# Kernel tuning notes

Measured on AMD Instinct MI355X. Metric: run time of the kernel, lower is better.

The kernel has to match this reference:

```python
import jax, jax.numpy as jnp
import numpy as np

EPS = 1e-6
NUM_HEADS = 8
ATTN_DIM = 64
LINEAR_DIM = 64


def _layer_norm(x, eps=EPS):
    # F.layer_norm without elementwise affine
    mu = jnp.mean(x, axis=-1, keepdims=True)
    var = jnp.mean(jnp.square(x - mu), axis=-1, keepdims=True)
    return (x - mu) * jax.lax.rsqrt(var + eps)


def setup_inputs() -> dict:
    key = jax.random.key(0)
    k1, k2, k3 = jax.random.split(key, 3)
    B, N, D = 4, 2048, 512
    x = jax.random.normal(k1, (B, N, D), dtype=jnp.float32)
    invalid_attn_mask = jnp.tril(jnp.ones((N, N), dtype=jnp.float32))  # causal
    uvqk = jax.random.normal(k2, (D, 2 * LINEAR_DIM * NUM_HEADS + 2 * ATTN_DIM * NUM_HEADS), dtype=jnp.float32) * 0.02
    o_w = jax.random.normal(k3, (D, LINEAR_DIM * NUM_HEADS), dtype=jnp.float32) * (1.0 / np.sqrt(D))  # torch Linear weight [out, in]
    o_b = jnp.zeros((D,), dtype=jnp.float32)
    return {"x": x, "invalid_attn_mask": invalid_attn_mask, "uvqk": uvqk, "o_w": o_w, "o_b": o_b}


def reference(x, invalid_attn_mask, uvqk, o_w, o_b):
    B, N, D = x.shape
    H, dA, dL = NUM_HEADS, ATTN_DIM, LINEAR_DIM
    normed_x = _layer_norm(x)
    # fused uvqk projection + silu activation
    proj = jax.nn.silu(jnp.einsum('bnd,de->bne', normed_x, uvqk))
    u, v, q, k = jnp.split(proj, [dL * H, 2 * dL * H, 2 * dL * H + dA * H], axis=-1)
    q_h = q.reshape(B, N, H, dA)
    k_h = k.reshape(B, N, H, dA)
    v_h = v.reshape(B, N, H, dL)
    # HSTU attention: SiLU(qk)/N, then mask multiply (no softmax)
    qk_attn = jnp.einsum('bnhd,bmhd->bhnm', q_h, k_h)
    qk_attn = jax.nn.silu(qk_attn) / N
    qk_attn = qk_attn * invalid_attn_mask[None, None, :, :]
    attn = jnp.einsum('bhnm,bmhd->bnhd', qk_attn, v_h).reshape(B, N, H * dL)
    a = _layer_norm(attn)
    o_input = u * a
    out = jnp.einsum('bnf,df->bnd', o_input, o_w) + o_b + x
    return out
```

## Files before the change

kernel.cpp:

```cpp
#include <hip/hip_runtime.h>
#include <cstdint>

#define NTOK 2048
#define DIM 512
#define EDIM 2048
#define BATCH 4
#define HEADS 8
#define BNROWS 8192
#define INV_N (1.0f/2048.0f)

typedef unsigned short u16;
typedef __bf16 bf16x8 __attribute__((ext_vector_type(8)));
typedef u16   u16x8  __attribute__((ext_vector_type(8)));
typedef u16   u16x4  __attribute__((ext_vector_type(4)));
typedef float f32x4  __attribute__((ext_vector_type(4)));

__device__ __forceinline__ u16 f2bf(float f) {
  union { float f; uint32_t u; } v; v.f = f;
  uint32_t r = v.u + 0x7FFFu + ((v.u >> 16) & 1u);
  return (u16)(r >> 16);
}
__device__ __forceinline__ u16 f2bfc(float f) {
  return __builtin_bit_cast(u16, (__bf16)f);
}
__device__ __forceinline__ float bf2f(u16 b) {
  union { uint32_t u; float f; } v; v.u = ((uint32_t)b) << 16;
  return v.f;
}
__device__ __forceinline__ bf16x8 ldb(const u16* p) {
  u16x8 r = *(const u16x8*)p;
  return __builtin_bit_cast(bf16x8, r);
}
#define MFMA16(a,b,c) __builtin_amdgcn_mfma_f32_16x16x32_bf16((a),(b),(c),0,0,0)

__device__ __forceinline__ float silu_nr(float s) {
  float e = __expf(-s);
  e = fminf(e, 1.7e38f);
  float d = 1.0f + e;
  float r = __builtin_amdgcn_rcpf(d);
  r = r * fmaf(-d, r, 2.0f);
  return s * r;
}

__device__ __forceinline__ void gload16(const u16* g, u16* lds) {
  __builtin_amdgcn_global_load_lds(
      (const __attribute__((address_space(1))) void*)g,
      (__attribute__((address_space(3))) void*)lds, 16, 0, 0);
}

__global__ __launch_bounds__(256) void k_pre(const float* __restrict__ uvqk,
                                             const float* __restrict__ ow,
                                             const float* __restrict__ x,
                                             u16* __restrict__ uvqk_t,
                                             u16* __restrict__ ow_bf,
                                             u16* __restrict__ xn) {
  __shared__ float tile[32][33];
  int bid = blockIdx.x, tid = threadIdx.x;
  if (bid < 1024) {
    int tx = tid & 31, ty = tid >> 5;
    int j0 = (bid & 63) * 32, k0 = (bid >> 6) * 32;
#pragma unroll
    for (int r = ty; r < 32; r += 8)
      tile[r][tx] = uvqk[(size_t)(k0 + r) * EDIM + j0 + tx];
    __syncthreads();
#pragma unroll
    for (int r = ty; r < 32; r += 8)
      uvqk_t[(size_t)(j0 + r) * DIM + k0 + tx] = f2bfc(tile[tx][r]);
  } else if (bid < 1280) {
    int i4 = (bid - 1024) * 1024 + tid * 4;
    float4 v = *(const float4*)(ow + i4);
    u16x4 o = {f2bfc(v.x), f2bfc(v.y), f2bfc(v.z), f2bfc(v.w)};
    *(u16x4*)(ow_bf + i4) = o;
  } else {
    int lane = tid & 63, wid = tid >> 6;
    size_t row = (size_t)(bid - 1280) * 4 + wid;
    const float* xr = x + row * DIM;
    float4 a = ((const float4*)xr)[lane * 2];
    float4 b = ((const float4*)xr)[lane * 2 + 1];
    float s = a.x + a.y + a.z + a.w + b.x + b.y + b.z + b.w;
#pragma unroll
    for (int o = 32; o; o >>= 1) s += __shfl_xor(s, o);
    float mu = s * (1.0f / DIM);
    float d[8] = {a.x - mu, a.y - mu, a.z - mu, a.w - mu,
                  b.x - mu, b.y - mu, b.z - mu, b.w - mu};
    float v = 0.f;
#pragma unroll
    for (int j = 0; j < 8; ++j) v += d[j] * d[j];
#pragma unroll
    for (int o = 32; o; o >>= 1) v += __shfl_xor(v, o);
    float rs = rsqrtf(v * (1.0f / DIM) + 1e-6f);
    u16x8 o8;
#pragma unroll
    for (int j = 0; j < 8; ++j) o8[j] = f2bfc(d[j] * rs);
    *(u16x8*)(xn + row * DIM + lane * 8) = o8;
  }
}

__global__ __launch_bounds__(256) void k_gemm1(const u16* __restrict__ A,
                                               const u16* __restrict__ Bt,
                                               u16* __restrict__ P,
                                               u16* __restrict__ vt) {
  __shared__ u16 As[128 * 64];
  __shared__ u16 Bs[128 * 64];
  int tid = threadIdx.x, lane = tid & 63, wid = tid >> 6;
  int lm = lane & 15, lg = lane >> 4;
  int wr = wid >> 1, wc = wid & 1;

  int bid = blockIdx.x;
  int xcd = bid & 7, idx = bid >> 3;
  int orig = xcd * 128 + idx;
  int r0 = (orig >> 4) * 128;
  int c0 = (orig & 15) * 128;

  int srow = wid * 8 + (lane >> 3);
  int scol = (lane & 7) * 8;

  f32x4 acc[4][4];
  f32x4 z = {0.f, 0.f, 0.f, 0.f};
#pragma unroll
  for (int mt = 0; mt < 4; ++mt)
#pragma unroll
    for (int nt = 0; nt < 4; ++nt) acc[mt][nt] = z;

  for (int ks = 0; ks < DIM / 64; ++ks) {
#pragma unroll
    for (int it = 0; it < 4; ++it) {
      gload16(A + (size_t)(r0 + it * 32 + srow) * DIM + ks * 64 + scol,
              As + it * 2048 + wid * 512);
      gload16(Bt + (size_t)(c0 + it * 32 + srow) * DIM + ks * 64 + scol,
              Bs + it * 2048 + wid * 512);
    }
    __syncthreads();

#pragma unroll
    for (int kk = 0; kk < 2; ++kk) {
      bf16x8 am[4], bn[4];
#pragma unroll
      for (int mt = 0; mt < 4; ++mt)
        am[mt] = ldb(&As[(wr * 64 + mt * 16 + lm) * 64 + kk * 32 + lg * 8]);
#pragma unroll
      for (int nt = 0; nt < 4; ++nt)
        bn[nt] = ldb(&Bs[(wc * 64 + nt * 16 + lm) * 64 + kk * 32 + lg * 8]);
#pragma unroll
      for (int mt = 0; mt < 4; ++mt)
#pragma unroll
        for (int nt = 0; nt < 4; ++nt)
          acc[mt][nt] = MFMA16(am[mt], bn[nt], acc[mt][nt]);
    }
    __syncthreads();
  }

  bool isv = (c0 >= 512) && (c0 < 1024);
  int btc = r0 >> 11;
  int nbw = (r0 & 2047) + wr * 64;
  int hv  = ((c0 - 512) >> 6) + wc;

  u16* ws = ((wid >> 1) ? Bs : As) + (wid & 1) * 4096;

#pragma unroll
  for (int mt = 0; mt < 4; ++mt)
#pragma unroll
    for (int nt = 0; nt < 4; ++nt) {
      u16 pv[4];
#pragma unroll
      for (int i = 0; i < 4; ++i) {
        pv[i] = f2bfc(silu_nr(acc[mt][nt][i]));
        int row = mt * 16 + lg * 4 + i;
        int col = nt * 16 + lm;
        ws[row * 64 + (col ^ ((row & 7) << 3))] = pv[i];
      }
      if (isv) {
        int e = nt * 16 + lm;
        int n = nbw + mt * 16 + lg * 4;
        u16x4 pk = {pv[0], pv[1], pv[2], pv[3]};
        *(u16x4*)(vt + ((size_t)(btc * 8 + hv) * 64 + e) * NTOK + n) = pk;
      }
    }

#pragma unroll
  for (int p = 0; p < 8; ++p) {
    int rrow = p * 8 + (lane >> 3);
    int rcol = (lane & 7) * 8;
    u16x8 vv = *(const u16x8*)&ws[rrow * 64 + (rcol ^ ((rrow & 7) << 3))];
    *(u16x8*)(P + (size_t)(r0 + wr * 64 + rrow) * EDIM + c0 + wc * 64 + rcol) = vv;
  }
}

__global__ __launch_bounds__(256) void k_attn(const u16* __restrict__ proj,
                                              const u16* __restrict__ vt,
                                              float* __restrict__ attn) {
  __shared__ u16 kv0[8192];
  __shared__ u16 kv1[8192];
  __shared__ u16 p_lds[4][16][64];
  int tid = threadIdx.x, lane = tid & 63, w = tid >> 6;
  int lm = lane & 15, lg = lane >> 4;

  int bid = blockIdx.x;
  int xcd = bid & 7, idx = bid >> 3;
  int qtile = 31 - (idx >> 2);
  int bh = (xcd << 2) + (idx & 3);
  int b = bh >> 3, h = bh & 7;
  int n0 = qtile * 64;
  int nrow = n0 + w * 16;
  int nlm = nrow + lm;

  const u16* pb = proj + (size_t)b * NTOK * EDIM;
  const u16* kb = pb + 1536 + h * 64;
  const u16* vb = vt + (size_t)bh * 64 * NTOK;

  f32x4 z = {0.f, 0.f, 0.f, 0.f};

  int sr = lane >> 3;
  int sc = ((lane & 7) ^ sr) * 8;
  const u16* ks0 = kb + (size_t)(w * 16 + sr) * EDIM + sc;
  const u16* ks1 = kb + (size_t)(w * 16 + 8 + sr) * EDIM + sc;
  const u16* vs0 = vb + (size_t)(w * 16 + sr) * NTOK + sc;
  const u16* vs1 = vb + (size_t)(w * 16 + 8 + sr) * NTOK + sc;

  const u16* qrow = pb + (size_t)nlm * EDIM + 1024 + h * 64 + lg * 8;
  bf16x8 qf0 = ldb(qrow), qf1 = ldb(qrow + 32);

  f32x4 acc[4];
#pragma unroll
  for (int et = 0; et < 4; ++et) acc[et] = z;

  int psw = (lm & 7) << 3;

  gload16(ks0, kv0 + (w * 16) * 64);
  gload16(ks1, kv0 + (w * 16 + 8) * 64);
  gload16(vs0, kv0 + 4096 + (w * 16) * 64);
  gload16(vs1, kv0 + 4096 + (w * 16 + 8) * 64);
  asm volatile("s_waitcnt vmcnt(0)" ::: "memory");
  __builtin_amdgcn_s_barrier();

  int ntl = qtile + 1;
  for (int t = 0; t < ntl; ++t) {
    const u16* kt = (t & 1) ? kv1 : kv0;
    const u16* vl = kt + 4096;
    if (t + 1 < ntl) {
      u16* kd = ((t + 1) & 1) ? kv1 : kv0;
      size_t ko = (size_t)(t + 1) * 64 * EDIM;
      size_t vo = (size_t)(t + 1) * 64;
      gload16(ks0 + ko, kd + (w * 16) * 64);
      gload16(ks1 + ko, kd + (w * 16 + 8) * 64);
      gload16(vs0 + vo, kd + 4096 + (w * 16) * 64);
      gload16(vs1 + vo, kd + 4096 + (w * 16 + 8) * 64);
    }
    bf16x8 kf[4][2];
#pragma unroll
    for (int mb = 0; mb < 4; ++mb)
#pragma unroll
      for (int kk = 0; kk < 2; ++kk)
        kf[mb][kk] = ldb(&kt[(mb * 16 + lm) * 64 +
                             ((kk * 32 + lg * 8) ^ ((lm & 7) << 3))]);
    if (t == qtile) {
#pragma unroll
      for (int mb = 0; mb < 4; ++mb) {
        f32x4 s = MFMA16(kf[mb][0], qf0, z);
        s = MFMA16(kf[mb][1], qf1, s);
        int m = t * 64 + mb * 16 + lg * 4;
        u16x4 pk;
#pragma unroll
        for (int i = 0; i < 4; ++i)
          pk[i] = (m + i <= nlm) ? f2bfc(silu_nr(s[i])) : (u16)0;
        *(u16x4*)&p_lds[w][lm][(mb * 16 + lg * 4) ^ psw] = pk;
      }
    } else {
#pragma unroll
      for (int mb = 0; mb < 4; ++mb) {
        f32x4 s = MFMA16(kf[mb][0], qf0, z);
        s = MFMA16(kf[mb][1], qf1, s);
        u16x4 pk;
#pragma unroll
        for (int i = 0; i < 4; ++i) pk[i] = f2bfc(silu_nr(s[i]));
        *(u16x4*)&p_lds[w][lm][(mb * 16 + lg * 4) ^ psw] = pk;
      }
    }
    bf16x8 vf[2][4];
#pragma unroll
    for (int kk = 0; kk < 2; ++kk)
#pragma unroll
      for (int et = 0; et < 4; ++et)
        vf[kk][et] = ldb(&vl[(et * 16 + lm) * 64 +
                             ((kk * 32 + lg * 8) ^ ((lm & 7) << 3))]);
    bf16x8 pf0 = ldb(&p_lds[w][lm][(lg * 8) ^ psw]);
    bf16x8 pf1 = ldb(&p_lds[w][lm][(32 + lg * 8) ^ psw]);
#pragma unroll
    for (int et = 0; et < 4; ++et) {
      acc[et] = MFMA16(pf0, vf[0][et], acc[et]);
      acc[et] = MFMA16(pf1, vf[1][et], acc[et]);
    }
    asm volatile("s_waitcnt vmcnt(0)" ::: "memory");
    __builtin_amdgcn_s_barrier();
  }

#pragma unroll
  for (int et = 0; et < 4; ++et)
#pragma unroll
    for (int i = 0; i < 4; ++i)
      attn[((size_t)b * NTOK + nrow + lg * 4 + i) * DIM +
           h * 64 + et * 16 + lm] = acc[et][i] * INV_N;
}

__global__ __launch_bounds__(256) void k_gemm2f(const float* __restrict__ attn,
                                                const u16* __restrict__ proj,
                                                const u16* __restrict__ Bw,
                                                const float* __restrict__ o_b,
                                                const float* __restrict__ x,
                                                float* __restrict__ out) {
  __shared__ u16 os[32 * 512];
  int tid = threadIdx.x, lane = tid & 63, w = tid >> 6;
  int lm = lane & 15, lg = lane >> 4;

  int bid = blockIdx.x;
  int xcd = bid & 7, idx = bid >> 3;
  int r0 = (xcd * 32 + idx) * 32;

#pragma unroll
  for (int rr = 0; rr < 8; ++rr) {
    int r = w * 8 + rr;
    const float* ar = attn + (size_t)(r0 + r) * DIM;
    float4 a = ((const float4*)ar)[lane * 2];
    float4 b = ((const float4*)ar)[lane * 2 + 1];
    float s = a.x + a.y + a.z + a.w + b.x + b.y + b.z + b.w;
#pragma unroll
    for (int o = 32; o; o >>= 1) s += __shfl_xor(s, o);
    float mu = s * (1.0f / DIM);
    float d[8] = {a.x - mu, a.y - mu, a.z - mu, a.w - mu,
                  b.x - mu, b.y - mu, b.z - mu, b.w - mu};
    float v = 0.f;
#pragma unroll
    for (int j = 0; j < 8; ++j) v += d[j] * d[j];
#pragma unroll
    for (int o = 32; o; o >>= 1) v += __shfl_xor(v, o);
    float rs = rsqrtf(v * (1.0f / DIM) + 1e-6f);
    u16x8 u8 = *(const u16x8*)(proj + (size_t)(r0 + r) * EDIM + lane * 8);
    u16x8 o8;
#pragma unroll
    for (int j = 0; j < 8; ++j) o8[j] = f2bf(bf2f(u8[j]) * (d[j] * rs));
    *(u16x8*)&os[r * 512 + ((lane * 8) ^ ((r & 7) << 3))] = o8;
  }
  __syncthreads();

  int cb = w * 128;
  f32x4 acc[2][8];
  f32x4 z = {0.f, 0.f, 0.f, 0.f};
#pragma unroll
  for (int mt = 0; mt < 2; ++mt)
#pragma unroll
    for (int nt = 0; nt < 8; ++nt) acc[mt][nt] = z;

#pragma unroll 2
  for (int kc = 0; kc < 16; ++kc) {
    bf16x8 af[2];
#pragma unroll
    for (int mt = 0; mt < 2; ++mt)
      af[mt] = ldb(&os[(mt * 16 + lm) * 512 +
                       ((kc * 32 + lg * 8) ^ ((lm & 7) << 3))]);
    bf16x8 bfr[8];
#pragma unroll
    for (int nt = 0; nt < 8; ++nt)
      bfr[nt] = ldb(Bw + (size_t)(cb + nt * 16 + lm) * DIM + kc * 32 + lg * 8);
#pragma unroll
    for (int mt = 0; mt < 2; ++mt)
#pragma unroll
      for (int nt = 0; nt < 8; ++nt)
        acc[mt][nt] = MFMA16(af[mt], bfr[nt], acc[mt][nt]);
  }

#pragma unroll
  for (int mt = 0; mt < 2; ++mt)
#pragma unroll
    for (int nt = 0; nt < 8; ++nt)
#pragma unroll
      for (int i = 0; i < 4; ++i) {
        size_t row = r0 + mt * 16 + lg * 4 + i;
        int col = cb + nt * 16 + lm;
        out[row * DIM + col] = acc[mt][nt][i] + o_b[col] + x[row * DIM + col];
      }
}

extern "C" void kernel_launch(void* const* d_in, const int* in_sizes, int n_in,
                              void* d_out, int out_size, void* d_ws, size_t ws_size,
                              hipStream_t stream) {
  const float* x    = (const float*)d_in[0];
  const float* uvqk = (const float*)d_in[2];
  const float* o_w  = (const float*)d_in[3];
  const float* o_b  = (const float*)d_in[4];
  float* out = (float*)d_out;

  u16* uvqk_t = (u16*)d_ws;
  u16* ow_bf  = uvqk_t + (size_t)EDIM * DIM;
  u16* xn     = ow_bf + (size_t)DIM * DIM;
  u16* proj   = xn + (size_t)BNROWS * DIM;
  float* attn = (float*)(proj + (size_t)BNROWS * EDIM);
  u16* o_in   = (u16*)(attn + (size_t)BNROWS * DIM);
  u16* vt     = o_in + (size_t)BNROWS * DIM;

  k_pre<<<dim3(3328), 256, 0, stream>>>(uvqk, o_w, x, uvqk_t, ow_bf, xn);
  k_gemm1<<<dim3(1024), 256, 0, stream>>>(xn, uvqk_t, proj, vt);
  k_attn<<<dim3(1024), 256, 0, stream>>>(proj, vt, attn);
  k_gemm2f<<<dim3(256), 256, 0, stream>>>(attn, proj, ow_bf, o_b, x, out);
}
```

Before: 112.6 us.

## Pair causal query tiles per attention block and halve gemm2 row tile

The attention kernel now processes 128-row query tiles, with each wave handling two 16-row sub-tiles. Each block runs two paired tiles (qt and 15-qt), so every block gets the same causal work and each K/V tile loaded into LDS is reused by more queries. MFMA priority is raised around the PV accumulation. The output GEMM drops to 16-row tiles and 512 blocks to raise parallelism, at the cost of reloading the o_w fragments more often.

```diff
diff --git a/kernel.cpp b/kernel.cpp
--- a/kernel.cpp
+++ b/kernel.cpp
@@ -191,18 +191,15 @@
                                               float* __restrict__ attn) {
   __shared__ u16 kv0[8192];
   __shared__ u16 kv1[8192];
-  __shared__ u16 p_lds[4][16][64];
+  __shared__ u16 p_lds[4][2][16][64];
   int tid = threadIdx.x, lane = tid & 63, w = tid >> 6;
   int lm = lane & 15, lg = lane >> 4;
 
   int bid = blockIdx.x;
   int xcd = bid & 7, idx = bid >> 3;
-  int qtile = 31 - (idx >> 2);
-  int bh = (xcd << 2) + (idx & 3);
+  int bh = (xcd << 2) + (idx >> 4);
+  int pairp = idx & 15;
   int b = bh >> 3, h = bh & 7;
-  int n0 = qtile * 64;
-  int nrow = n0 + w * 16;
-  int nlm = nrow + lm;
 
   const u16* pb = proj + (size_t)b * NTOK * EDIM;
   const u16* kb = pb + 1536 + h * 64;
@@ -217,89 +214,120 @@
   const u16* vs0 = vb + (size_t)(w * 16 + sr) * NTOK + sc;
   const u16* vs1 = vb + (size_t)(w * 16 + 8 + sr) * NTOK + sc;
 
-  const u16* qrow = pb + (size_t)nlm * EDIM + 1024 + h * 64 + lg * 8;
-  bf16x8 qf0 = ldb(qrow), qf1 = ldb(qrow + 32);
-
-  f32x4 acc[4];
-#pragma unroll
-  for (int et = 0; et < 4; ++et) acc[et] = z;
-
   int psw = (lm & 7) << 3;
 
-  gload16(ks0, kv0 + (w * 16) * 64);
-  gload16(ks1, kv0 + (w * 16 + 8) * 64);
-  gload16(vs0, kv0 + 4096 + (w * 16) * 64);
-  gload16(vs1, kv0 + 4096 + (w * 16 + 8) * 64);
-  asm volatile("s_waitcnt vmcnt(0)" ::: "memory");
-  __builtin_amdgcn_s_barrier();
-
-  int ntl = qtile + 1;
-  for (int t = 0; t < ntl; ++t) {
-    const u16* kt = (t & 1) ? kv1 : kv0;
-    const u16* vl = kt + 4096;
-    if (t + 1 < ntl) {
-      u16* kd = ((t + 1) & 1) ? kv1 : kv0;
-      size_t ko = (size_t)(t + 1) * 64 * EDIM;
-      size_t vo = (size_t)(t + 1) * 64;
-      gload16(ks0 + ko, kd + (w * 16) * 64);
-      gload16(ks1 + ko, kd + (w * 16 + 8) * 64);
-      gload16(vs0 + vo, kd + 4096 + (w * 16) * 64);
-      gload16(vs1 + vo, kd + 4096 + (w * 16 + 8) * 64);
-    }
-    bf16x8 kf[4][2];
-#pragma unroll
-    for (int mb = 0; mb < 4; ++mb)
-#pragma unroll
-      for (int kk = 0; kk < 2; ++kk)
-        kf[mb][kk] = ldb(&kt[(mb * 16 + lm) * 64 +
-                             ((kk * 32 + lg * 8) ^ ((lm & 7) << 3))]);
-    if (t == qtile) {
-#pragma unroll
-      for (int mb = 0; mb < 4; ++mb) {
-        f32x4 s = MFMA16(kf[mb][0], qf0, z);
-        s = MFMA16(kf[mb][1], qf1, s);
-        int m = t * 64 + mb * 16 + lg * 4;
-        u16x4 pk;
-#pragma unroll
-        for (int i = 0; i < 4; ++i)
-          pk[i] = (m + i <= nlm) ? f2bfc(silu_nr(s[i])) : (u16)0;
-        *(u16x4*)&p_lds[w][lm][(mb * 16 + lg * 4) ^ psw] = pk;
-      }
-    } else {
-#pragma unroll
-      for (int mb = 0; mb < 4; ++mb) {
-        f32x4 s = MFMA16(kf[mb][0], qf0, z);
-        s = MFMA16(kf[mb][1], qf1, s);
-        u16x4 pk;
-#pragma unroll
-        for (int i = 0; i < 4; ++i) pk[i] = f2bfc(silu_nr(s[i]));
-        *(u16x4*)&p_lds[w][lm][(mb * 16 + lg * 4) ^ psw] = pk;
-      }
-    }
-    bf16x8 vf[2][4];
-#pragma unroll
-    for (int kk = 0; kk < 2; ++kk)
-#pragma unroll
-      for (int et = 0; et < 4; ++et)
-        vf[kk][et] = ldb(&vl[(et * 16 + lm) * 64 +
-                             ((kk * 32 + lg * 8) ^ ((lm & 7) << 3))]);
-    bf16x8 pf0 = ldb(&p_lds[w][lm][(lg * 8) ^ psw]);
-    bf16x8 pf1 = ldb(&p_lds[w][lm][(32 + lg * 8) ^ psw]);
-#pragma unroll
-    for (int et = 0; et < 4; ++et) {
-      acc[et] = MFMA16(pf0, vf[0][et], acc[et]);
-      acc[et] = MFMA16(pf1, vf[1][et], acc[et]);
-    }
+#pragma unroll
+  for (int ph = 0; ph < 2; ++ph) {
+    int qt = ph ? pairp : (15 - pairp);
+    int n0 = qt * 128;
+    int nw = n0 + w * 32;
+
+    bf16x8 qf[2][2];
+#pragma unroll
+    for (int qs = 0; qs < 2; ++qs) {
+      const u16* qrow = pb + (size_t)(nw + qs * 16 + lm) * EDIM + 1024 + h * 64 + lg * 8;
+      qf[qs][0] = ldb(qrow);
+      qf[qs][1] = ldb(qrow + 32);
+    }
+
+    f32x4 acc[2][4];
+#pragma unroll
+    for (int qs = 0; qs < 2; ++qs)
+#pragma unroll
+      for (int et = 0; et < 4; ++et) acc[qs][et] = z;
+
+    gload16(ks0, kv0 + (w * 16) * 64);
+    gload16(ks1, kv0 + (w * 16 + 8) * 64);
+    gload16(vs0, kv0 + 4096 + (w * 16) * 64);
+    gload16(vs1, kv0 + 4096 + (w * 16 + 8) * 64);
     asm volatile("s_waitcnt vmcnt(0)" ::: "memory");
     __builtin_amdgcn_s_barrier();
-  }
-
-#pragma unroll
-  for (int et = 0; et < 4; ++et)
-#pragma unroll
-    for (int i = 0; i < 4; ++i)
-      attn[((size_t)b * NTOK + nrow + lg * 4 + i) * DIM +
-           h * 64 + et * 16 + lm] = acc[et][i] * INV_N;
+
+    int ntl = 2 * qt + 2;
+    for (int t = 0; t < ntl; ++t) {
+      const u16* kt = (t & 1) ? kv1 : kv0;
+      const u16* vl = kt + 4096;
+      if (t + 1 < ntl) {
+        u16* kd = ((t + 1) & 1) ? kv1 : kv0;
+        size_t ko = (size_t)(t + 1) * 64 * EDIM;
+        size_t vo = (size_t)(t + 1) * 64;
+        gload16(ks0 + ko, kd + (w * 16) * 64);
+        gload16(ks1 + ko, kd + (w * 16 + 8) * 64);
+        gload16(vs0 + vo, kd + 4096 + (w * 16) * 64);
+        gload16(vs1 + vo, kd + 4096 + (w * 16 + 8) * 64);
+      }
+      int m0 = t * 64;
+      bf16x8 kf[4][2];
+#pragma unroll
+      for (int mb = 0; mb < 4; ++mb)
+#pragma unroll
+        for (int kk = 0; kk < 2; ++kk)
+          kf[mb][kk] = ldb(&kt[(mb * 16 + lm) * 64 +
+                               ((kk * 32 + lg * 8) ^ ((lm & 7) << 3))]);
+#pragma unroll
+      for (int qs = 0; qs < 2; ++qs) {
+        int nwqs = nw + qs * 16;
+        if (m0 <= nwqs + 15) {
+          int nlm = nwqs + lm;
+          if (m0 + 63 <= nwqs) {
+#pragma unroll
+            for (int mb = 0; mb < 4; ++mb) {
+              f32x4 s = MFMA16(kf[mb][0], qf[qs][0], z);
+              s = MFMA16(kf[mb][1], qf[qs][1], s);
+              u16x4 pk;
+#pragma unroll
+              for (int i = 0; i < 4; ++i) pk[i] = f2bfc(silu_nr(s[i]));
+              *(u16x4*)&p_lds[w][qs][lm][(mb * 16 + lg * 4) ^ psw] = pk;
+            }
+          } else {
+#pragma unroll
+            for (int mb = 0; mb < 4; ++mb) {
+              f32x4 s = MFMA16(kf[mb][0], qf[qs][0], z);
+              s = MFMA16(kf[mb][1], qf[qs][1], s);
+              int m = m0 + mb * 16 + lg * 4;
+              u16x4 pk;
+#pragma unroll
+              for (int i = 0; i < 4; ++i)
+                pk[i] = (m + i <= nlm) ? f2bfc(silu_nr(s[i])) : (u16)0;
+              *(u16x4*)&p_lds[w][qs][lm][(mb * 16 + lg * 4) ^ psw] = pk;
+            }
+          }
+        }
+      }
+      bf16x8 vf[2][4];
+#pragma unroll
+      for (int kk = 0; kk < 2; ++kk)
+#pragma unroll
+        for (int et = 0; et < 4; ++et)
+          vf[kk][et] = ldb(&vl[(et * 16 + lm) * 64 +
+                               ((kk * 32 + lg * 8) ^ ((lm & 7) << 3))]);
+#pragma unroll
+      for (int qs = 0; qs < 2; ++qs) {
+        if (m0 <= nw + qs * 16 + 15) {
+          bf16x8 pf0 = ldb(&p_lds[w][qs][lm][(lg * 8) ^ psw]);
+          bf16x8 pf1 = ldb(&p_lds[w][qs][lm][(32 + lg * 8) ^ psw]);
+          __builtin_amdgcn_s_setprio(1);
+#pragma unroll
+          for (int et = 0; et < 4; ++et) {
+            acc[qs][et] = MFMA16(pf0, vf[0][et], acc[qs][et]);
+            acc[qs][et] = MFMA16(pf1, vf[1][et], acc[qs][et]);
+          }
+          __builtin_amdgcn_s_setprio(0);
+        }
+      }
+      asm volatile("s_waitcnt vmcnt(0)" ::: "memory");
+      __builtin_amdgcn_s_barrier();
+    }
+
+#pragma unroll
+    for (int qs = 0; qs < 2; ++qs)
+#pragma unroll
+      for (int et = 0; et < 4; ++et)
+#pragma unroll
+        for (int i = 0; i < 4; ++i)
+          attn[((size_t)b * NTOK + nw + qs * 16 + lg * 4 + i) * DIM +
+               h * 64 + et * 16 + lm] = acc[qs][et][i] * INV_N;
+  }
 }
 
 __global__ __launch_bounds__(256) void k_gemm2f(const float* __restrict__ attn,
@@ -308,17 +336,17 @@
                                                 const float* __restrict__ o_b,
                                                 const float* __restrict__ x,
                                                 float* __restrict__ out) {
-  __shared__ u16 os[32 * 512];
+  __shared__ u16 os[16 * 512];
   int tid = threadIdx.x, lane = tid & 63, w = tid >> 6;
   int lm = lane & 15, lg = lane >> 4;
 
   int bid = blockIdx.x;
   int xcd = bid & 7, idx = bid >> 3;
-  int r0 = (xcd * 32 + idx) * 32;
-
-#pragma unroll
-  for (int rr = 0; rr < 8; ++rr) {
-    int r = w * 8 + rr;
+  int r0 = (xcd * 64 + idx) * 16;
+
+#pragma unroll
+  for (int rr = 0; rr < 4; ++rr) {
+    int r = w * 4 + rr;
     const float* ar = attn + (size_t)(r0 + r) * DIM;
     float4 a = ((const float4*)ar)[lane * 2];
     float4 b = ((const float4*)ar)[lane * 2 + 1];
@@ -343,41 +371,31 @@
   __syncthreads();
 
   int cb = w * 128;
-  f32x4 acc[2][8];
+  f32x4 acc[8];
   f32x4 z = {0.f, 0.f, 0.f, 0.f};
 #pragma unroll
-  for (int mt = 0; mt < 2; ++mt)
-#pragma unroll
-    for (int nt = 0; nt < 8; ++nt) acc[mt][nt] = z;
+  for (int nt = 0; nt < 8; ++nt) acc[nt] = z;
 
 #pragma unroll 2
   for (int kc = 0; kc < 16; ++kc) {
-    bf16x8 af[2];
-#pragma unroll
-    for (int mt = 0; mt < 2; ++mt)
-      af[mt] = ldb(&os[(mt * 16 + lm) * 512 +
-                       ((kc * 32 + lg * 8) ^ ((lm & 7) << 3))]);
+    bf16x8 af = ldb(&os[lm * 512 + ((kc * 32 + lg * 8) ^ ((lm & 7) << 3))]);
     bf16x8 bfr[8];
 #pragma unroll
     for (int nt = 0; nt < 8; ++nt)
       bfr[nt] = ldb(Bw + (size_t)(cb + nt * 16 + lm) * DIM + kc * 32 + lg * 8);
 #pragma unroll
-    for (int mt = 0; mt < 2; ++mt)
-#pragma unroll
-      for (int nt = 0; nt < 8; ++nt)
-        acc[mt][nt] = MFMA16(af[mt], bfr[nt], acc[mt][nt]);
-  }
-
-#pragma unroll
-  for (int mt = 0; mt < 2; ++mt)
-#pragma unroll
     for (int nt = 0; nt < 8; ++nt)
-#pragma unroll
-      for (int i = 0; i < 4; ++i) {
-        size_t row = r0 + mt * 16 + lg * 4 + i;
-        int col = cb + nt * 16 + lm;
-        out[row * DIM + col] = acc[mt][nt][i] + o_b[col] + x[row * DIM + col];
-      }
+      acc[nt] = MFMA16(af, bfr[nt], acc[nt]);
+  }
+
+#pragma unroll
+  for (int nt = 0; nt < 8; ++nt)
+#pragma unroll
+    for (int i = 0; i < 4; ++i) {
+      size_t row = r0 + lg * 4 + i;
+      int col = cb + nt * 16 + lm;
+      out[row * DIM + col] = acc[nt][i] + o_b[col] + x[row * DIM + col];
+    }
 }
 
 extern "C" void kernel_launch(void* const* d_in, const int* in_sizes, int n_in,
@@ -399,6 +417,6 @@
 
   k_pre<<<dim3(3328), 256, 0, stream>>>(uvqk, o_w, x, uvqk_t, ow_bf, xn);
   k_gemm1<<<dim3(1024), 256, 0, stream>>>(xn, uvqk_t, proj, vt);
-  k_attn<<<dim3(1024), 256, 0, stream>>>(proj, vt, attn);
-  k_gemm2f<<<dim3(256), 256, 0, stream>>>(attn, proj, ow_bf, o_b, x, out);
-}
+  k_attn<<<dim3(512), 256, 0, stream>>>(proj, vt, attn);
+  k_gemm2f<<<dim3(512), 256, 0, stream>>>(attn, proj, ow_bf, o_b, x, out);
+}
```

After: 159.4 us. +41.6%, slower.
